# Optimization experiments

Measured on AMD Instinct MI355X. Metric: run time of the kernel, lower is better.

Reference implementation:

```python
import jax, jax.numpy as jnp
import numpy as np

B, S, D, H = 2, 4096, 768, 12
HD = D // H
SCALE = HD ** -0.5


def setup_inputs() -> dict:
    key = jax.random.key(0)
    k_x, k_wq, k_bq, k_wp, k_bp = jax.random.split(key, 5)
    lim_qkv = (1.0 / D) ** 0.5
    lim_p = (1.0 / D) ** 0.5
    return {
        "x": jax.random.normal(k_x, (B, S, D), dtype=jnp.float32),
        "qkv_w": jax.random.uniform(k_wq, (3 * D, D), dtype=jnp.float32, minval=-lim_qkv, maxval=lim_qkv),
        "qkv_b": jax.random.uniform(k_bq, (3 * D,), dtype=jnp.float32, minval=-lim_qkv, maxval=lim_qkv),
        "proj_w": jax.random.uniform(k_wp, (D, D), dtype=jnp.float32, minval=-lim_p, maxval=lim_p),
        "proj_b": jax.random.uniform(k_bp, (D,), dtype=jnp.float32, minval=-lim_p, maxval=lim_p),
    }


def reference(x, qkv_w, qkv_b, proj_w, proj_b):
    b, s, _ = x.shape
    qkv = x @ qkv_w.T + qkv_b                      # [b, s, 3D]
    q, k, v = jnp.split(qkv, 3, axis=-1)           # each [b, s, D]
    # [b, s, D] -> [b, H, s, HD]
    def to_heads(t):
        return t.reshape(b, s, H, HD).transpose(0, 2, 1, 3)
    q, k, v = to_heads(q), to_heads(k), to_heads(v)
    attn = jnp.einsum("bhqd,bhkd->bhqk", q, k) * SCALE   # [b, H, s, s]
    attn = jax.nn.softmax(attn, axis=-1)
    out = jnp.einsum("bhqk,bhkd->bhqd", attn, v)         # [b, H, s, HD]
    out = out.transpose(0, 2, 1, 3).reshape(b, s, D)
    return out @ proj_w.T + proj_b
```

## Files before the change

### kernel.cpp

```cpp
#include <hip/hip_runtime.h>
#include <hip/hip_bf16.h>


#define B_ 2
#define S_ 4096
#define D_ 768
#define H_ 12
#define HD_ 64
#define TD_ (3 * D_)
#define QKD_ (2 * D_)

static constexpr float LOG2E = 1.4426950408889634f;

typedef __bf16 bf16x8 __attribute__((ext_vector_type(8)));
typedef unsigned short ushortx8 __attribute__((ext_vector_type(8)));
typedef unsigned short ushortx4 __attribute__((ext_vector_type(4)));
typedef float floatx4 __attribute__((ext_vector_type(4)));

__device__ inline unsigned short f2bf(float f) {
  return __builtin_bit_cast(unsigned short, (__bf16)f);
}
__device__ inline float bf2f(unsigned short u) {
  return __uint_as_float(((unsigned int)u) << 16);
}
__device__ inline void glds16(const unsigned short* g, unsigned short* l) {
  __builtin_amdgcn_global_load_lds(
      (const __attribute__((address_space(1))) unsigned int*)g,
      (__attribute__((address_space(3))) unsigned int*)l, 16, 0, 0);
}

__global__ __launch_bounds__(256)
void gemm_qkv(const float* __restrict__ A,
              const float* __restrict__ W,
              const float* __restrict__ bias,
              unsigned short* __restrict__ qkbuf,
              unsigned short* __restrict__ vT) {
  constexpr int BM = 128, BK = 64, PAD = 8;
  constexpr int K = D_;
  __shared__ __attribute__((aligned(16))) unsigned short As[BM][BK + PAD];
  __shared__ __attribute__((aligned(16))) unsigned short Ws[BM][BK + PAD];

  const int tid = threadIdx.x;
  const int lane = tid & 63;
  const int wid = tid >> 6;
  const int wm = wid >> 1;
  const int wn = wid & 1;
  const int m0 = blockIdx.y * BM;
  const int n0 = blockIdx.x * BM;
  const int lr = lane & 15;
  const int lk = (lane >> 4) * 8;
  const int ro = (lane >> 4) * 4;

  floatx4 acc[4][4];
#pragma unroll
  for (int m = 0; m < 4; ++m)
#pragma unroll
    for (int n = 0; n < 4; ++n) acc[m][n] = (floatx4){0.f, 0.f, 0.f, 0.f};

  for (int kb = 0; kb < K; kb += BK) {
#pragma unroll
    for (int it = 0; it < 8; ++it) {
      int c = tid + it * 256;
      int row = c >> 4, ch = c & 15;
      floatx4 v = *reinterpret_cast<const floatx4*>(&W[(size_t)(n0 + row) * K + kb + ch * 4]);
      ushortx4 o;
#pragma unroll
      for (int j = 0; j < 4; ++j) o[j] = f2bf(v[j]);
      *reinterpret_cast<ushortx4*>(&Ws[row][ch * 4]) = o;
      floatx4 va = *reinterpret_cast<const floatx4*>(&A[(size_t)(m0 + row) * K + kb + ch * 4]);
      ushortx4 oa;
#pragma unroll
      for (int j = 0; j < 4; ++j) oa[j] = f2bf(va[j]);
      *reinterpret_cast<ushortx4*>(&As[row][ch * 4]) = oa;
    }
    __syncthreads();

#pragma unroll
    for (int ks = 0; ks < 2; ++ks) {
      bf16x8 af[4], bfr[4];
#pragma unroll
      for (int m = 0; m < 4; ++m)
        af[m] = *reinterpret_cast<const bf16x8*>(&As[wm * 64 + m * 16 + lr][ks * 32 + lk]);
#pragma unroll
      for (int n = 0; n < 4; ++n)
        bfr[n] = *reinterpret_cast<const bf16x8*>(&Ws[wn * 64 + n * 16 + lr][ks * 32 + lk]);
#pragma unroll
      for (int m = 0; m < 4; ++m)
#pragma unroll
        for (int n = 0; n < 4; ++n)
          acc[m][n] = __builtin_amdgcn_mfma_f32_16x16x32_bf16(af[m], bfr[n], acc[m][n], 0, 0, 0);
    }
    __syncthreads();
  }

  const bool is_v = (n0 >= QKD_);
#pragma unroll
  for (int n = 0; n < 4; ++n) {
    int col = n0 + wn * 64 + n * 16 + lr;
    float bv = bias[col];
#pragma unroll
    for (int m = 0; m < 4; ++m) {
      int row = m0 + wm * 64 + m * 16 + ro;
      if (is_v) {
        int dcol = col - QKD_;
        int hh = dcol >> 6, dd = dcol & 63;
        int bb = row >> 12, s = row & (S_ - 1);
        int s5 = s & 31;
        int spos = (s & ~31) + ((s5 >> 2) & 3) * 8 + ((s5 >> 4) & 1) * 4;
        ushortx4 o4;
#pragma unroll
        for (int i = 0; i < 4; ++i) o4[i] = f2bf(acc[m][n][i] + bv);
        *reinterpret_cast<ushortx4*>(
            &vT[(size_t)((bb * H_ + hh) * 64 + dd) * S_ + spos]) = o4;
      } else {
#pragma unroll
        for (int i = 0; i < 4; ++i)
          qkbuf[(size_t)(row + i) * QKD_ + col] = f2bf(acc[m][n][i] + bv);
      }
    }
  }
}

__global__ __launch_bounds__(256)
void gemm_proj(const unsigned short* __restrict__ A,
               const float* __restrict__ W,
               const float* __restrict__ bias,
               float* __restrict__ C,
               int M, int N, int K) {
  constexpr int BM = 128, BK = 64, PAD = 8;
  __shared__ __attribute__((aligned(16))) unsigned short As[BM][BK + PAD];
  __shared__ __attribute__((aligned(16))) unsigned short Ws[BM][BK + PAD];

  const int tid = threadIdx.x;
  const int lane = tid & 63;
  const int wid = tid >> 6;
  const int wm = wid >> 1;
  const int wn = wid & 1;
  const int m0 = blockIdx.y * BM;
  const int n0 = blockIdx.x * BM;
  const int lr = lane & 15;
  const int lk = (lane >> 4) * 8;
  const int ro = (lane >> 4) * 4;

  floatx4 acc[4][4];
#pragma unroll
  for (int m = 0; m < 4; ++m)
#pragma unroll
    for (int n = 0; n < 4; ++n) acc[m][n] = (floatx4){0.f, 0.f, 0.f, 0.f};

  for (int kb = 0; kb < K; kb += BK) {
#pragma unroll
    for (int it = 0; it < 8; ++it) {
      int c = tid + it * 256;
      int row = c >> 4, ch = c & 15;
      floatx4 v = *reinterpret_cast<const floatx4*>(&W[(size_t)(n0 + row) * K + kb + ch * 4]);
      ushortx4 o;
#pragma unroll
      for (int j = 0; j < 4; ++j) o[j] = f2bf(v[j]);
      *reinterpret_cast<ushortx4*>(&Ws[row][ch * 4]) = o;
    }
#pragma unroll
    for (int it = 0; it < 4; ++it) {
      int c = tid + it * 256;
      int row = c >> 3, ch = c & 7;
      *reinterpret_cast<ushortx8*>(&As[row][ch * 8]) =
          *reinterpret_cast<const ushortx8*>(&A[(size_t)(m0 + row) * K + kb + ch * 8]);
    }
    __syncthreads();

#pragma unroll
    for (int ks = 0; ks < 2; ++ks) {
      bf16x8 af[4], bfr[4];
#pragma unroll
      for (int m = 0; m < 4; ++m)
        af[m] = *reinterpret_cast<const bf16x8*>(&As[wm * 64 + m * 16 + lr][ks * 32 + lk]);
#pragma unroll
      for (int n = 0; n < 4; ++n)
        bfr[n] = *reinterpret_cast<const bf16x8*>(&Ws[wn * 64 + n * 16 + lr][ks * 32 + lk]);
#pragma unroll
      for (int m = 0; m < 4; ++m)
#pragma unroll
        for (int n = 0; n < 4; ++n)
          acc[m][n] = __builtin_amdgcn_mfma_f32_16x16x32_bf16(af[m], bfr[n], acc[m][n], 0, 0, 0);
    }
    __syncthreads();
  }

#pragma unroll
  for (int n = 0; n < 4; ++n) {
    int col = n0 + wn * 64 + n * 16 + lr;
    float bv = bias[col];
#pragma unroll
    for (int m = 0; m < 4; ++m) {
      int row = m0 + wm * 64 + m * 16 + ro;
#pragma unroll
      for (int i = 0; i < 4; ++i)
        C[(size_t)(row + i) * N + col] = acc[m][n][i] + bv;
    }
  }
}

__global__ __launch_bounds__(256)
void attn_kernel(const unsigned short* __restrict__ qkbuf,
                 const unsigned short* __restrict__ vT,
                 unsigned short* __restrict__ out) {
  constexpr int QB = 128, KVB = 64, NT = S_ / KVB;
  __shared__ __attribute__((aligned(16))) unsigned short Ks[2][KVB][64];
  __shared__ __attribute__((aligned(16))) unsigned short Vt[2][HD_][64];

  const int tid = threadIdx.x;
  const int lane = tid & 63;
  const int wid = tid >> 6;
  const int q0 = blockIdx.x * QB;
  const int h = blockIdx.y;
  const int b = blockIdx.z;
  const int lr = lane & 15;
  const int g = lane >> 4;
  const int e8 = lr & 7;
  const int wq = wid * 32;

  const unsigned short* Qg = qkbuf + (size_t)b * S_ * QKD_ + (size_t)h * HD_;
  const unsigned short* Kg = Qg + D_;
  const unsigned short* Vg = vT + (size_t)(b * H_ + h) * HD_ * S_;

  const int srow = lane >> 3;
  const int sch = lane & 7;

  bf16x8 qf[2][2];
#pragma unroll
  for (int qt = 0; qt < 2; ++qt)
#pragma unroll
    for (int ks = 0; ks < 2; ++ks) {
      ushortx8 r = *reinterpret_cast<const ushortx8*>(
          &Qg[(size_t)(q0 + wq + qt * 16 + lr) * QKD_ + ks * 32 + g * 8]);
      bf16x8 q;
#pragma unroll
      for (int j = 0; j < 8; ++j) q[j] = (__bf16)(bf2f(r[j]) * (0.125f * LOG2E));
      qf[qt][ks] = q;
    }

  floatx4 lrv[2] = {(floatx4){0.f, 0.f, 0.f, 0.f}, (floatx4){0.f, 0.f, 0.f, 0.f}};
  floatx4 oacc[2][4];
#pragma unroll
  for (int qt = 0; qt < 2; ++qt)
#pragma unroll
    for (int dt = 0; dt < 4; ++dt) oacc[qt][dt] = (floatx4){0.f, 0.f, 0.f, 0.f};

  const unsigned short* kp0 = Kg + (size_t)(wid * 16 + srow) * QKD_ + (sch ^ srow) * 8;
  const unsigned short* kp1 = kp0 + (size_t)8 * QKD_;
  const unsigned short* vp0 = Vg + (size_t)(wid * 16 + srow) * S_ + (sch ^ srow) * 8;
  const unsigned short* vp1 = vp0 + (size_t)8 * S_;

#define STAGE(BUF) do { \
    glds16(kp0, &Ks[BUF][wid * 16][0]); \
    glds16(kp1, &Ks[BUF][wid * 16 + 8][0]); \
    glds16(vp0, &Vt[BUF][wid * 16][0]); \
    glds16(vp1, &Vt[BUF][wid * 16 + 8][0]); \
    kp0 += (size_t)KVB * QKD_; kp1 += (size_t)KVB * QKD_; \
    vp0 += KVB; vp1 += KVB; } while (0)

#define COMPUTE(BUF) do { \
    bf16x8 kf[4][2], vf[2][4]; \
    _Pragma("unroll") \
    for (int kt = 0; kt < 4; ++kt) \
      _Pragma("unroll") \
      for (int ks = 0; ks < 2; ++ks) \
        kf[kt][ks] = *reinterpret_cast<const bf16x8*>( \
            &Ks[BUF][kt * 16 + lr][(((ks << 2) + g) ^ e8) * 8]); \
    _Pragma("unroll") \
    for (int ks = 0; ks < 2; ++ks) \
      _Pragma("unroll") \
      for (int dt = 0; dt < 4; ++dt) \
        vf[ks][dt] = *reinterpret_cast<const bf16x8*>( \
            &Vt[BUF][dt * 16 + lr][(((ks << 2) + g) ^ e8) * 8]); \
    _Pragma("unroll") \
    for (int qt = 0; qt < 2; ++qt) { \
      floatx4 sc[4]; \
      _Pragma("unroll") \
      for (int kt = 0; kt < 4; ++kt) { \
        floatx4 c = (floatx4){0.f, 0.f, 0.f, 0.f}; \
        _Pragma("unroll") \
        for (int ks = 0; ks < 2; ++ks) \
          c = __builtin_amdgcn_mfma_f32_16x16x32_bf16(kf[kt][ks], qf[qt][ks], c, 0, 0, 0); \
        sc[kt] = c; \
      } \
      _Pragma("unroll") \
      for (int kt = 0; kt < 4; ++kt) \
        _Pragma("unroll") \
        for (int i = 0; i < 4; ++i) \
          sc[kt][i] = __builtin_amdgcn_exp2f(sc[kt][i]); \
      lrv[qt] += (sc[0] + sc[1]) + (sc[2] + sc[3]); \
      bf16x8 pf0, pf1; \
      _Pragma("unroll") \
      for (int j = 0; j < 8; ++j) { \
        pf0[j] = (__bf16)sc[(j >> 2)][j & 3]; \
        pf1[j] = (__bf16)sc[2 + (j >> 2)][j & 3]; \
      } \
      _Pragma("unroll") \
      for (int dt = 0; dt < 4; ++dt) \
        oacc[qt][dt] = __builtin_amdgcn_mfma_f32_16x16x32_bf16(vf[0][dt], pf0, oacc[qt][dt], 0, 0, 0); \
      _Pragma("unroll") \
      for (int dt = 0; dt < 4; ++dt) \
        oacc[qt][dt] = __builtin_amdgcn_mfma_f32_16x16x32_bf16(vf[1][dt], pf1, oacc[qt][dt], 0, 0, 0); \
    } } while (0)

  STAGE(0);
  for (int t = 0; t < NT; t += 2) {
    __syncthreads();
    STAGE(1);
    COMPUTE(0);
    __syncthreads();
    if (t + 2 < NT) STAGE(0);
    COMPUTE(1);
  }
#undef STAGE
#undef COMPUTE

#pragma unroll
  for (int qt = 0; qt < 2; ++qt) {
    float l = (lrv[qt][0] + lrv[qt][1]) + (lrv[qt][2] + lrv[qt][3]);
    l += __shfl_xor(l, 16, 64);
    l += __shfl_xor(l, 32, 64);
    float inv = __builtin_amdgcn_rcpf(l);
    size_t rowbase = ((size_t)b * S_ + q0 + wq + qt * 16 + lr) * D_ + h * HD_;
#pragma unroll
    for (int dt = 0; dt < 4; ++dt) {
      ushortx4 o4;
#pragma unroll
      for (int i = 0; i < 4; ++i) o4[i] = f2bf(oacc[qt][dt][i] * inv);
      *reinterpret_cast<ushortx4*>(&out[rowbase + dt * 16 + 4 * g]) = o4;
    }
  }
}

extern "C" void kernel_launch(void* const* d_in, const int* in_sizes, int n_in,
                              void* d_out, int out_size, void* d_ws, size_t ws_size,
                              hipStream_t stream) {
  const float* x      = (const float*)d_in[0];
  const float* qkv_w  = (const float*)d_in[1];
  const float* qkv_b  = (const float*)d_in[2];
  const float* proj_w = (const float*)d_in[3];
  const float* proj_b = (const float*)d_in[4];
  float* out = (float*)d_out;

  unsigned short* qkbuf   = (unsigned short*)d_ws;
  unsigned short* vTbuf   = qkbuf + (size_t)B_ * S_ * QKD_;
  unsigned short* attnbuf = vTbuf + (size_t)B_ * H_ * HD_ * S_;

  dim3 blk(256);
  gemm_qkv<<<dim3(TD_ / 128, (B_ * S_) / 128), blk, 0, stream>>>(
      x, qkv_w, qkv_b, qkbuf, vTbuf);
  attn_kernel<<<dim3(S_ / 128, H_, B_), blk, 0, stream>>>(qkbuf, vTbuf, attnbuf);
  gemm_proj<<<dim3(D_ / 128, (B_ * S_) / 128), blk, 0, stream>>>(
      attnbuf, proj_w, proj_b, out, B_ * S_, D_, D_);
}
```

Baseline: 234.3 us.

## Pre-convert to bf16, use async LDS GEMM loads, split attention KV range

Three small kernels now convert x and both weight matrices to bf16 up front. The two GEMMs are merged into one templated bf16 kernel that stages tiles with global_load_lds and an XOR-swizzled LDS layout instead of converting fp32 in registers. The projection GEMM now uses a narrower 64-column tile, which doubles its block count. When the workspace is large enough, attention splits the KV sequence in two across more blocks, writes fp32 partial outputs and row sums, and a combine kernel merges them. This trades extra launches and partial-result memory traffic for better GEMM load efficiency and more attention parallelism.

Measured after the change: 216.2 us. 7.7% less time.

```diff
diff --git a/kernel.cpp b/kernel.cpp
--- a/kernel.cpp
+++ b/kernel.cpp
@@ -30,15 +30,29 @@
 }
 
 __global__ __launch_bounds__(256)
-void gemm_qkv(const float* __restrict__ A,
-              const float* __restrict__ W,
-              const float* __restrict__ bias,
-              unsigned short* __restrict__ qkbuf,
-              unsigned short* __restrict__ vT) {
-  constexpr int BM = 128, BK = 64, PAD = 8;
-  constexpr int K = D_;
-  __shared__ __attribute__((aligned(16))) unsigned short As[BM][BK + PAD];
-  __shared__ __attribute__((aligned(16))) unsigned short Ws[BM][BK + PAD];
+void cvt_bf16(const float* __restrict__ src, unsigned short* __restrict__ dst, int n4) {
+  int idx = blockIdx.x * 256 + threadIdx.x;
+  if (idx < n4) {
+    floatx4 v = *reinterpret_cast<const floatx4*>(&src[(size_t)idx * 4]);
+    ushortx4 o;
+#pragma unroll
+    for (int j = 0; j < 4; ++j) o[j] = f2bf(v[j]);
+    *reinterpret_cast<ushortx4*>(&dst[(size_t)idx * 4]) = o;
+  }
+}
+
+template <int NFR, bool QKV_EPI>
+__global__ __launch_bounds__(256)
+void gemm_bf16(const unsigned short* __restrict__ A,
+               const unsigned short* __restrict__ W,
+               const float* __restrict__ bias,
+               float* __restrict__ Cf,
+               unsigned short* __restrict__ qkbuf,
+               unsigned short* __restrict__ vT,
+               int M, int N, int K) {
+  constexpr int BM = 128, BN = NFR * 32, BK = 64;
+  __shared__ __attribute__((aligned(16))) unsigned short As[BM][BK];
+  __shared__ __attribute__((aligned(16))) unsigned short Ws[BN][BK];
 
   const int tid = threadIdx.x;
   const int lane = tid & 63;
@@ -46,165 +60,94 @@
   const int wm = wid >> 1;
   const int wn = wid & 1;
   const int m0 = blockIdx.y * BM;
-  const int n0 = blockIdx.x * BM;
+  const int n0 = blockIdx.x * BN;
   const int lr = lane & 15;
-  const int lk = (lane >> 4) * 8;
-  const int ro = (lane >> 4) * 4;
-
-  floatx4 acc[4][4];
+  const int g = lane >> 4;
+  const int e8 = lr & 7;
+  const int ro = g * 4;
+  const int srow = lane >> 3;
+  const int sch = lane & 7;
+
+  floatx4 acc[4][NFR];
 #pragma unroll
   for (int m = 0; m < 4; ++m)
 #pragma unroll
-    for (int n = 0; n < 4; ++n) acc[m][n] = (floatx4){0.f, 0.f, 0.f, 0.f};
+    for (int n = 0; n < NFR; ++n) acc[m][n] = (floatx4){0.f, 0.f, 0.f, 0.f};
 
   for (int kb = 0; kb < K; kb += BK) {
 #pragma unroll
-    for (int it = 0; it < 8; ++it) {
-      int c = tid + it * 256;
-      int row = c >> 4, ch = c & 15;
-      floatx4 v = *reinterpret_cast<const floatx4*>(&W[(size_t)(n0 + row) * K + kb + ch * 4]);
-      ushortx4 o;
-#pragma unroll
-      for (int j = 0; j < 4; ++j) o[j] = f2bf(v[j]);
-      *reinterpret_cast<ushortx4*>(&Ws[row][ch * 4]) = o;
-      floatx4 va = *reinterpret_cast<const floatx4*>(&A[(size_t)(m0 + row) * K + kb + ch * 4]);
-      ushortx4 oa;
-#pragma unroll
-      for (int j = 0; j < 4; ++j) oa[j] = f2bf(va[j]);
-      *reinterpret_cast<ushortx4*>(&As[row][ch * 4]) = oa;
+    for (int c = 0; c < 4; ++c) {
+      int seg = wid * 4 + c;
+      int row = seg * 8 + srow;
+      glds16(&A[(size_t)(m0 + row) * K + kb + ((sch ^ srow) << 3)], &As[seg * 8][0]);
+    }
+#pragma unroll
+    for (int c = 0; c < NFR; ++c) {
+      int seg = wid * NFR + c;
+      int row = seg * 8 + srow;
+      glds16(&W[(size_t)(n0 + row) * K + kb + ((sch ^ srow) << 3)], &Ws[seg * 8][0]);
     }
     __syncthreads();
 
 #pragma unroll
     for (int ks = 0; ks < 2; ++ks) {
-      bf16x8 af[4], bfr[4];
+      int ch = ((ks << 2) + g) ^ e8;
+      bf16x8 af[4], bfr[NFR];
 #pragma unroll
       for (int m = 0; m < 4; ++m)
-        af[m] = *reinterpret_cast<const bf16x8*>(&As[wm * 64 + m * 16 + lr][ks * 32 + lk]);
-#pragma unroll
-      for (int n = 0; n < 4; ++n)
-        bfr[n] = *reinterpret_cast<const bf16x8*>(&Ws[wn * 64 + n * 16 + lr][ks * 32 + lk]);
+        af[m] = *reinterpret_cast<const bf16x8*>(&As[wm * 64 + m * 16 + lr][ch << 3]);
+#pragma unroll
+      for (int n = 0; n < NFR; ++n)
+        bfr[n] = *reinterpret_cast<const bf16x8*>(&Ws[wn * (NFR * 16) + n * 16 + lr][ch << 3]);
 #pragma unroll
       for (int m = 0; m < 4; ++m)
 #pragma unroll
-        for (int n = 0; n < 4; ++n)
+        for (int n = 0; n < NFR; ++n)
           acc[m][n] = __builtin_amdgcn_mfma_f32_16x16x32_bf16(af[m], bfr[n], acc[m][n], 0, 0, 0);
     }
     __syncthreads();
   }
 
-  const bool is_v = (n0 >= QKD_);
-#pragma unroll
-  for (int n = 0; n < 4; ++n) {
-    int col = n0 + wn * 64 + n * 16 + lr;
+#pragma unroll
+  for (int n = 0; n < NFR; ++n) {
+    int col = n0 + wn * (NFR * 16) + n * 16 + lr;
     float bv = bias[col];
 #pragma unroll
     for (int m = 0; m < 4; ++m) {
       int row = m0 + wm * 64 + m * 16 + ro;
-      if (is_v) {
-        int dcol = col - QKD_;
-        int hh = dcol >> 6, dd = dcol & 63;
-        int bb = row >> 12, s = row & (S_ - 1);
-        int s5 = s & 31;
-        int spos = (s & ~31) + ((s5 >> 2) & 3) * 8 + ((s5 >> 4) & 1) * 4;
-        ushortx4 o4;
-#pragma unroll
-        for (int i = 0; i < 4; ++i) o4[i] = f2bf(acc[m][n][i] + bv);
-        *reinterpret_cast<ushortx4*>(
-            &vT[(size_t)((bb * H_ + hh) * 64 + dd) * S_ + spos]) = o4;
+      if constexpr (QKV_EPI) {
+        if (col >= QKD_) {
+          int dcol = col - QKD_;
+          int hh = dcol >> 6, dd = dcol & 63;
+          int bb = row >> 12, s = row & (S_ - 1);
+          int s5 = s & 31;
+          int spos = (s & ~31) + ((s5 >> 2) & 3) * 8 + ((s5 >> 4) & 1) * 4;
+          ushortx4 o4;
+#pragma unroll
+          for (int i = 0; i < 4; ++i) o4[i] = f2bf(acc[m][n][i] + bv);
+          *reinterpret_cast<ushortx4*>(
+              &vT[(size_t)((bb * H_ + hh) * 64 + dd) * S_ + spos]) = o4;
+        } else {
+#pragma unroll
+          for (int i = 0; i < 4; ++i)
+            qkbuf[(size_t)(row + i) * QKD_ + col] = f2bf(acc[m][n][i] + bv);
+        }
       } else {
 #pragma unroll
         for (int i = 0; i < 4; ++i)
-          qkbuf[(size_t)(row + i) * QKD_ + col] = f2bf(acc[m][n][i] + bv);
+          Cf[(size_t)(row + i) * N + col] = acc[m][n][i] + bv;
       }
     }
   }
 }
 
-__global__ __launch_bounds__(256)
-void gemm_proj(const unsigned short* __restrict__ A,
-               const float* __restrict__ W,
-               const float* __restrict__ bias,
-               float* __restrict__ C,
-               int M, int N, int K) {
-  constexpr int BM = 128, BK = 64, PAD = 8;
-  __shared__ __attribute__((aligned(16))) unsigned short As[BM][BK + PAD];
-  __shared__ __attribute__((aligned(16))) unsigned short Ws[BM][BK + PAD];
-
-  const int tid = threadIdx.x;
-  const int lane = tid & 63;
-  const int wid = tid >> 6;
-  const int wm = wid >> 1;
-  const int wn = wid & 1;
-  const int m0 = blockIdx.y * BM;
-  const int n0 = blockIdx.x * BM;
-  const int lr = lane & 15;
-  const int lk = (lane >> 4) * 8;
-  const int ro = (lane >> 4) * 4;
-
-  floatx4 acc[4][4];
-#pragma unroll
-  for (int m = 0; m < 4; ++m)
-#pragma unroll
-    for (int n = 0; n < 4; ++n) acc[m][n] = (floatx4){0.f, 0.f, 0.f, 0.f};
-
-  for (int kb = 0; kb < K; kb += BK) {
-#pragma unroll
-    for (int it = 0; it < 8; ++it) {
-      int c = tid + it * 256;
-      int row = c >> 4, ch = c & 15;
-      floatx4 v = *reinterpret_cast<const floatx4*>(&W[(size_t)(n0 + row) * K + kb + ch * 4]);
-      ushortx4 o;
-#pragma unroll
-      for (int j = 0; j < 4; ++j) o[j] = f2bf(v[j]);
-      *reinterpret_cast<ushortx4*>(&Ws[row][ch * 4]) = o;
-    }
-#pragma unroll
-    for (int it = 0; it < 4; ++it) {
-      int c = tid + it * 256;
-      int row = c >> 3, ch = c & 7;
-      *reinterpret_cast<ushortx8*>(&As[row][ch * 8]) =
-          *reinterpret_cast<const ushortx8*>(&A[(size_t)(m0 + row) * K + kb + ch * 8]);
-    }
-    __syncthreads();
-
-#pragma unroll
-    for (int ks = 0; ks < 2; ++ks) {
-      bf16x8 af[4], bfr[4];
-#pragma unroll
-      for (int m = 0; m < 4; ++m)
-        af[m] = *reinterpret_cast<const bf16x8*>(&As[wm * 64 + m * 16 + lr][ks * 32 + lk]);
-#pragma unroll
-      for (int n = 0; n < 4; ++n)
-        bfr[n] = *reinterpret_cast<const bf16x8*>(&Ws[wn * 64 + n * 16 + lr][ks * 32 + lk]);
-#pragma unroll
-      for (int m = 0; m < 4; ++m)
-#pragma unroll
-        for (int n = 0; n < 4; ++n)
-          acc[m][n] = __builtin_amdgcn_mfma_f32_16x16x32_bf16(af[m], bfr[n], acc[m][n], 0, 0, 0);
-    }
-    __syncthreads();
-  }
-
-#pragma unroll
-  for (int n = 0; n < 4; ++n) {
-    int col = n0 + wn * 64 + n * 16 + lr;
-    float bv = bias[col];
-#pragma unroll
-    for (int m = 0; m < 4; ++m) {
-      int row = m0 + wm * 64 + m * 16 + ro;
-#pragma unroll
-      for (int i = 0; i < 4; ++i)
-        C[(size_t)(row + i) * N + col] = acc[m][n][i] + bv;
-    }
-  }
-}
-
+template <int NSPLIT>
 __global__ __launch_bounds__(256)
 void attn_kernel(const unsigned short* __restrict__ qkbuf,
                  const unsigned short* __restrict__ vT,
-                 unsigned short* __restrict__ out) {
-  constexpr int QB = 128, KVB = 64, NT = S_ / KVB;
+                 unsigned short* __restrict__ outb,
+                 float* __restrict__ po, float* __restrict__ pl) {
+  constexpr int QB = 128, KVB = 64, NT = S_ / KVB / NSPLIT;
   __shared__ __attribute__((aligned(16))) unsigned short Ks[2][KVB][64];
   __shared__ __attribute__((aligned(16))) unsigned short Vt[2][HD_][64];
 
@@ -213,7 +156,9 @@
   const int wid = tid >> 6;
   const int q0 = blockIdx.x * QB;
   const int h = blockIdx.y;
-  const int b = blockIdx.z;
+  const int b = (NSPLIT == 1) ? blockIdx.z : (blockIdx.z >> 1);
+  const int sp = (NSPLIT == 1) ? 0 : (blockIdx.z & 1);
+  const int kvbase = sp * (S_ / NSPLIT);
   const int lr = lane & 15;
   const int g = lane >> 4;
   const int e8 = lr & 7;
@@ -246,9 +191,9 @@
 #pragma unroll
     for (int dt = 0; dt < 4; ++dt) oacc[qt][dt] = (floatx4){0.f, 0.f, 0.f, 0.f};
 
-  const unsigned short* kp0 = Kg + (size_t)(wid * 16 + srow) * QKD_ + (sch ^ srow) * 8;
+  const unsigned short* kp0 = Kg + (size_t)(kvbase + wid * 16 + srow) * QKD_ + ((sch ^ srow) << 3);
   const unsigned short* kp1 = kp0 + (size_t)8 * QKD_;
-  const unsigned short* vp0 = Vg + (size_t)(wid * 16 + srow) * S_ + (sch ^ srow) * 8;
+  const unsigned short* vp0 = Vg + (size_t)(wid * 16 + srow) * S_ + kvbase + ((sch ^ srow) << 3);
   const unsigned short* vp1 = vp0 + (size_t)8 * S_;
 
 #define STAGE(BUF) do { \
@@ -321,16 +266,49 @@
     float l = (lrv[qt][0] + lrv[qt][1]) + (lrv[qt][2] + lrv[qt][3]);
     l += __shfl_xor(l, 16, 64);
     l += __shfl_xor(l, 32, 64);
-    float inv = __builtin_amdgcn_rcpf(l);
-    size_t rowbase = ((size_t)b * S_ + q0 + wq + qt * 16 + lr) * D_ + h * HD_;
-#pragma unroll
-    for (int dt = 0; dt < 4; ++dt) {
-      ushortx4 o4;
-#pragma unroll
-      for (int i = 0; i < 4; ++i) o4[i] = f2bf(oacc[qt][dt][i] * inv);
-      *reinterpret_cast<ushortx4*>(&out[rowbase + dt * 16 + 4 * g]) = o4;
-    }
-  }
+    int q = q0 + wq + qt * 16 + lr;
+    if constexpr (NSPLIT == 1) {
+      float inv = __builtin_amdgcn_rcpf(l);
+      size_t rowbase = ((size_t)b * S_ + q) * D_ + h * HD_;
+#pragma unroll
+      for (int dt = 0; dt < 4; ++dt) {
+        ushortx4 o4;
+#pragma unroll
+        for (int i = 0; i < 4; ++i) o4[i] = f2bf(oacc[qt][dt][i] * inv);
+        *reinterpret_cast<ushortx4*>(&outb[rowbase + dt * 16 + 4 * g]) = o4;
+      }
+    } else {
+      size_t rowbase = ((size_t)(sp * B_ + b) * S_ + q) * D_ + h * HD_;
+#pragma unroll
+      for (int dt = 0; dt < 4; ++dt)
+        *reinterpret_cast<floatx4*>(&po[rowbase + dt * 16 + 4 * g]) = oacc[qt][dt];
+      if (lane < 16)
+        pl[((size_t)((sp * B_ + b) * H_ + h)) * S_ + q] = l;
+    }
+  }
+}
+
+__global__ __launch_bounds__(256)
+void combine_kernel(const float* __restrict__ po, const float* __restrict__ pl,
+                    unsigned short* __restrict__ attnbuf) {
+  int gid = blockIdx.x * 256 + threadIdx.x;
+  int d4 = gid & 15;
+  int rest = gid >> 4;
+  int h = rest % H_;
+  int bq = rest / H_;
+  size_t o0 = (size_t)bq * D_ + h * 64 + d4 * 4;
+  const size_t half = (size_t)B_ * S_ * D_;
+  floatx4 a = *reinterpret_cast<const floatx4*>(&po[o0]);
+  floatx4 c = *reinterpret_cast<const floatx4*>(&po[o0 + half]);
+  int q = bq & (S_ - 1);
+  int b = bq >> 12;
+  float l = pl[(size_t)(b * H_ + h) * S_ + q] +
+            pl[(size_t)((B_ + b) * H_ + h) * S_ + q];
+  float inv = __builtin_amdgcn_rcpf(l);
+  ushortx4 o;
+#pragma unroll
+  for (int i = 0; i < 4; ++i) o[i] = f2bf((a[i] + c[i]) * inv);
+  *reinterpret_cast<ushortx4*>(&attnbuf[o0]) = o;
 }
 
 extern "C" void kernel_launch(void* const* d_in, const int* in_sizes, int n_in,
@@ -346,11 +324,32 @@
   unsigned short* qkbuf   = (unsigned short*)d_ws;
   unsigned short* vTbuf   = qkbuf + (size_t)B_ * S_ * QKD_;
   unsigned short* attnbuf = vTbuf + (size_t)B_ * H_ * HD_ * S_;
+  unsigned short* xbf     = attnbuf + (size_t)B_ * S_ * D_;
+  unsigned short* wqkvbf  = xbf + (size_t)B_ * S_ * D_;
+  unsigned short* wprojbf = wqkvbf + (size_t)TD_ * D_;
+  float* po = (float*)(wprojbf + (size_t)D_ * D_);
+  float* pl = po + (size_t)2 * B_ * S_ * D_;
+
+  const size_t need = ((char*)(pl + (size_t)2 * B_ * H_ * S_)) - (char*)d_ws;
+  const bool split = ws_size >= need;
 
   dim3 blk(256);
-  gemm_qkv<<<dim3(TD_ / 128, (B_ * S_) / 128), blk, 0, stream>>>(
-      x, qkv_w, qkv_b, qkbuf, vTbuf);
-  attn_kernel<<<dim3(S_ / 128, H_, B_), blk, 0, stream>>>(qkbuf, vTbuf, attnbuf);
-  gemm_proj<<<dim3(D_ / 128, (B_ * S_) / 128), blk, 0, stream>>>(
-      attnbuf, proj_w, proj_b, out, B_ * S_, D_, D_);
-}
+  cvt_bf16<<<dim3((B_ * S_ * D_ / 4 + 255) / 256), blk, 0, stream>>>(x, xbf, B_ * S_ * D_ / 4);
+  cvt_bf16<<<dim3((TD_ * D_ / 4 + 255) / 256), blk, 0, stream>>>(qkv_w, wqkvbf, TD_ * D_ / 4);
+  cvt_bf16<<<dim3((D_ * D_ / 4 + 255) / 256), blk, 0, stream>>>(proj_w, wprojbf, D_ * D_ / 4);
+
+  gemm_bf16<4, true><<<dim3(TD_ / 128, (B_ * S_) / 128), blk, 0, stream>>>(
+      xbf, wqkvbf, qkv_b, nullptr, qkbuf, vTbuf, B_ * S_, TD_, D_);
+
+  if (split) {
+    attn_kernel<2><<<dim3(S_ / 128, H_, B_ * 2), blk, 0, stream>>>(
+        qkbuf, vTbuf, attnbuf, po, pl);
+    combine_kernel<<<dim3(B_ * S_ * H_ * 16 / 256), blk, 0, stream>>>(po, pl, attnbuf);
+  } else {
+    attn_kernel<1><<<dim3(S_ / 128, H_, B_), blk, 0, stream>>>(
+        qkbuf, vTbuf, attnbuf, nullptr, nullptr);
+  }
+
+  gemm_bf16<2, false><<<dim3(D_ / 64, (B_ * S_) / 128), blk, 0, stream>>>(
+      attnbuf, wprojbf, proj_b, out, nullptr, nullptr, B_ * S_, D_, D_);
+}
```
